# Kernel optimization log

Measured on AMD Instinct MI355X. Metric: run time of the kernel, lower is better.

The kernel has to match this reference:

```python
import jax, jax.numpy as jnp
import numpy as np
from jax import lax

B, T, D, E, N, P, S, NCLS, NBLK = 64, 16384, 128, 256, 8, 16, 1024, 18, 3
EPS = 1e-5


def setup_inputs() -> dict:
    key = jax.random.key(0)
    ks = jax.random.split(key, 20)
    inp = {
        'inputs': jax.random.normal(ks[0], (B, T, 6), jnp.float32),
        'acc_w': jax.random.normal(ks[1], (D // 2, 3, P), jnp.float32) * 0.1,
        'acc_b': jnp.zeros((D // 2,), jnp.float32),
        'gyro_w': jax.random.normal(ks[2], (D // 2, 3, P), jnp.float32) * 0.1,
        'gyro_b': jnp.zeros((D // 2,), jnp.float32),
        'pos_emb': jax.random.normal(ks[3], (S, D), jnp.float32),
        'ln_g': jnp.ones((NBLK, D), jnp.float32),
        'ln_b': jnp.zeros((NBLK, D), jnp.float32),
        'pc1_w': jax.random.normal(ks[4], (NBLK, E, D), jnp.float32) * 0.05,
        'pc1_b': jnp.zeros((NBLK, E), jnp.float32),
        'dw_w': jax.random.normal(ks[5], (NBLK, E, 5), jnp.float32) * 0.1,
        'dw_b': jnp.zeros((NBLK, E), jnp.float32),
        'bn_g': jnp.ones((NBLK, E), jnp.float32),
        'bn_b': jnp.zeros((NBLK, E), jnp.float32),
        'bn_mean': jnp.zeros((NBLK, E), jnp.float32),
        'bn_var': jnp.ones((NBLK, E), jnp.float32),
        'Ap': -0.5 * jnp.ones((NBLK, E), jnp.float32),
        'Bp': jax.random.normal(ks[6], (NBLK, E, N), jnp.float32) * 0.1,
        'Cp': jax.random.normal(ks[7], (NBLK, E, N), jnp.float32) * 0.1,
        'Dp': jax.random.normal(ks[8], (NBLK, E), jnp.float32) * 0.1,
        'pc2_w': jax.random.normal(ks[9], (NBLK, D, E), jnp.float32) * 0.05,
        'pc2_b': jnp.zeros((NBLK, D), jnp.float32),
        'fln_g': jnp.ones((D,), jnp.float32),
        'fln_b': jnp.zeros((D,), jnp.float32),
        'hw1': jax.random.normal(ks[10], (D, 2 * D), jnp.float32) * 0.05,
        'hb1': jnp.zeros((2 * D,), jnp.float32),
        'hw2': jax.random.normal(ks[11], (2 * D, NCLS), jnp.float32) * 0.05,
        'hb2': jnp.zeros((NCLS,), jnp.float32),
    }
    return inp


def _layernorm(x, g, b):
    m = x.mean(-1, keepdims=True)
    v = ((x - m) ** 2).mean(-1, keepdims=True)
    return (x - m) * lax.rsqrt(v + EPS) * g + b


def _conv1d(x, w, b, stride):
    # x [B,C,L], w [O,I,K]
    y = lax.conv_general_dilated(x, w, (stride,), 'VALID',
                                 dimension_numbers=('NCH', 'OIH', 'NCH'))
    return y + b[None, :, None]


def _mamba(x, pc1_w, pc1_b, dw_w, dw_b, bn_g, bn_b, bn_mean, bn_var,
           Ap, Bp, Cp, Dp, pc2_w, pc2_b):
    # x: [B,S,D]
    xc = jax.nn.silu(jnp.einsum('bsd,ed->bse', x, pc1_w) + pc1_b)  # [B,S,E]
    xt = jnp.swapaxes(xc, 1, 2)  # [B,E,S]
    # depthwise conv k=5, pad=2, groups=E
    xl = lax.conv_general_dilated(xt, dw_w[:, None, :], (1,), [(2, 2)],
                                  feature_group_count=E,
                                  dimension_numbers=('NCH', 'OIH', 'NCH'))
    xl = xl + dw_b[None, :, None]
    # BatchNorm1d (eval mode, running stats)
    scale = bn_g * lax.rsqrt(bn_var + EPS)
    xl = (xl - bn_mean[None, :, None]) * scale[None, :, None] + bn_b[None, :, None]
    xl = jax.nn.silu(xl)
    x_local = jnp.swapaxes(xl, 1, 2)  # [B,S,E]
    # SSM scan: h = exp(A)*h + x_t * B ; y = sum(C*h) + D*x_t
    A_exp = jnp.exp(Ap)  # [E]

    def step(h, xt_):
        # h [B,E,N], xt_ [B,E]
        h = A_exp[None, :, None] * h + xt_[..., None] * Bp[None]
        y = jnp.einsum('ben,en->be', h, Cp) + Dp * xt_
        return h, y

    h0 = jnp.zeros((x_local.shape[0], E, N), x_local.dtype)
    _, ys = lax.scan(step, h0, jnp.swapaxes(x_local, 0, 1))  # ys [S,B,E]
    out = jnp.swapaxes(ys, 0, 1)  # [B,S,E]
    out = jnp.einsum('bse,de->bsd', out, pc2_w) + pc2_b
    return out


def reference(inputs, acc_w, acc_b, gyro_w, gyro_b, pos_emb,
              ln_g, ln_b, pc1_w, pc1_b, dw_w, dw_b, bn_g, bn_b, bn_mean, bn_var,
              Ap, Bp, Cp, Dp, pc2_w, pc2_b, fln_g, fln_b, hw1, hb1, hw2, hb2):
    acc = jnp.swapaxes(inputs[:, :, :3], 1, 2)   # [B,3,T]
    gyro = jnp.swapaxes(inputs[:, :, 3:], 1, 2)  # [B,3,T]
    acc_p = jnp.swapaxes(_conv1d(acc, acc_w, acc_b, 16), 1, 2)    # [B,S,D/2]
    gyro_p = jnp.swapaxes(_conv1d(gyro, gyro_w, gyro_b, 16), 1, 2)
    x = jnp.concatenate([acc_p, gyro_p], axis=2)  # [B,S,D]
    x = x + pos_emb[None]
    for i in range(NBLK):
        y = _layernorm(x, ln_g[i], ln_b[i])
        y = _mamba(y, pc1_w[i], pc1_b[i], dw_w[i], dw_b[i], bn_g[i], bn_b[i],
                   bn_mean[i], bn_var[i], Ap[i], Bp[i], Cp[i], Dp[i],
                   pc2_w[i], pc2_b[i])
        x = y + x
    x = _layernorm(x, fln_g, fln_b)
    x = x.mean(axis=1)  # [B,D]
    h = jax.nn.silu(x @ hw1 + hb1)
    logits = h @ hw2 + hb2
    return jax.nn.softmax(logits, axis=-1)
```

## Files before the change

kernel.cpp:

```cpp
#include <hip/hip_runtime.h>
#include <hip/hip_bf16.h>

#define BB 64
#define TT 16384
#define DD 128
#define EE 256
#define NN 8
#define SS 1024
#define NCLS 18
#define NBLK 3
#define EPSV 1e-5f

typedef __bf16 bf16x8 __attribute__((ext_vector_type(8)));
typedef __bf16 bf16x4 __attribute__((ext_vector_type(4)));
typedef float f32x4 __attribute__((ext_vector_type(4)));
typedef unsigned short ushort_t;

__device__ __forceinline__ float silu_f(float z) {
    return z * __builtin_amdgcn_rcpf(1.0f + __expf(-z));
}
__device__ __forceinline__ unsigned int bfbits(float v) {
    return (unsigned int)__builtin_bit_cast(unsigned short, (__bf16)v);
}
__device__ __forceinline__ float bflow(unsigned int u) {
    return (float)__builtin_bit_cast(__bf16, (unsigned short)(u & 0xffffu));
}
__device__ __forceinline__ float bfhigh(unsigned int u) {
    return (float)__builtin_bit_cast(__bf16, (unsigned short)(u >> 16));
}

__global__ __launch_bounds__(256) void k_pack(
    const float* __restrict__ w1, const float* __restrict__ w2,
    const float* __restrict__ dw_w, const float* __restrict__ dw_b,
    const float* __restrict__ bn_g, const float* __restrict__ bn_b,
    const float* __restrict__ bn_mean, const float* __restrict__ bn_var,
    const float* __restrict__ Ap, const float* __restrict__ Bp,
    const float* __restrict__ Cp, const float* __restrict__ Dp,
    ushort_t* __restrict__ wpk1, ushort_t* __restrict__ wpk2,
    float* __restrict__ sparm) {
    const int t0 = blockIdx.x * 256 + threadIdx.x;
    if (t0 >= 24576) {
        const int t = t0 - 24576;
        if (t >= 768) return;
        const int le = t;
        const float scale = bn_g[le] * rsqrtf(bn_var[le] + EPSV);
        float cb = 0.0f;
#pragma unroll
        for (int n = 0; n < 8; ++n) cb += Cp[le * 8 + n] * Bp[le * 8 + n];
        float* dst = sparm + (size_t)le * 12;
        dst[0] = dw_w[le * 5 + 0] * scale;
        dst[1] = dw_w[le * 5 + 1] * scale;
        dst[2] = dw_w[le * 5 + 2] * scale;
        dst[3] = dw_w[le * 5 + 3] * scale;
        dst[4] = dw_w[le * 5 + 4] * scale;
        dst[5] = (dw_b[le] - bn_mean[le]) * scale + bn_b[le];
        dst[6] = __expf(Ap[le]);
        dst[7] = cb;
        dst[8] = Dp[le];
        dst[9] = 0.0f; dst[10] = 0.0f; dst[11] = 0.0f;
        return;
    }
    const float* src;
    uint4* dst;
    if (t0 < 12288) {
        const int L = t0 >> 12;
        const int r = t0 & 4095;
        const int ks = r >> 10;
        const int r2 = r & 1023;
        const int nf = r2 >> 6;
        const int lane = r2 & 63;
        const int col = nf * 16 + (lane & 15);
        const int k0 = ks * 32 + (lane >> 4) * 8;
        src = w1 + ((size_t)L * EE + col) * DD + k0;
        dst = (uint4*)wpk1 + t0;
    } else {
        const int t = t0 - 12288;
        const int L = t >> 12;
        const int r = t & 4095;
        const int ks = r >> 9;
        const int r2 = r & 511;
        const int nf = r2 >> 6;
        const int lane = r2 & 63;
        const int col = nf * 16 + (lane & 15);
        const int k0 = ks * 32 + (lane >> 4) * 8;
        src = w2 + ((size_t)L * DD + col) * EE + k0;
        dst = (uint4*)wpk2 + t;
    }
    const float4 a = ((const float4*)src)[0];
    const float4 b = ((const float4*)src)[1];
    bf16x8 pk;
    pk[0] = (__bf16)a.x; pk[1] = (__bf16)a.y; pk[2] = (__bf16)a.z; pk[3] = (__bf16)a.w;
    pk[4] = (__bf16)b.x; pk[5] = (__bf16)b.y; pk[6] = (__bf16)b.z; pk[7] = (__bf16)b.w;
    *dst = __builtin_bit_cast(uint4, pk);
}

__device__ __forceinline__ void xt_store(ushort_t* xt16, int row, int col,
                                         ushort_t val) {
    xt16[row * 128 + (((col >> 3) ^ (row & 7)) << 3) + (col & 7)] = val;
}

template <int MROWS, int NT>
__device__ __forceinline__ void ln_pc1_tail(
    char* smem, const int tid,
    const float* __restrict__ lng, const float* __restrict__ lnb,
    const ushort_t* __restrict__ wpk, const float* __restrict__ bias1,
    __bf16* __restrict__ xcT, const int bidx, const int sg0) {
    constexpr int TPR = NT / MROWS;
    constexpr int CPT = 16 / TPR;
    const uint4* xt = (const uint4*)smem;
    uint4* A2 = (uint4*)(smem + MROWS * 256);

    {
        const int row = tid / TPR;
        const int q = tid % TPR;
        float v[CPT * 8];
#pragma unroll
        for (int i = 0; i < CPT; ++i) {
            const uint4 tv4 = xt[row * 16 + ((q * CPT + i) ^ (row & 7))];
            const bf16x8 tv = __builtin_bit_cast(bf16x8, tv4);
#pragma unroll
            for (int e2 = 0; e2 < 8; ++e2) v[i * 8 + e2] = (float)tv[e2];
        }
        float s1 = 0.0f, s2 = 0.0f;
#pragma unroll
        for (int i = 0; i < CPT * 8; ++i) { s1 += v[i]; s2 += v[i] * v[i]; }
        s1 += __shfl_xor(s1, 1); s2 += __shfl_xor(s2, 1);
        s1 += __shfl_xor(s1, 2); s2 += __shfl_xor(s2, 2);
        const float mean = s1 * (1.0f / 128.0f);
        const float rstd = rsqrtf(s2 * (1.0f / 128.0f) - mean * mean + EPSV);
        const float4* gp4 = (const float4*)lng;
        const float4* bp4 = (const float4*)lnb;
#pragma unroll
        for (int c = 0; c < CPT; ++c) {
            const int ci = q * CPT + c;
            float4 g0 = gp4[ci * 2], g1 = gp4[ci * 2 + 1];
            float4 b0 = bp4[ci * 2], b1 = bp4[ci * 2 + 1];
            const float gg[8] = {g0.x, g0.y, g0.z, g0.w, g1.x, g1.y, g1.z, g1.w};
            const float bb2[8] = {b0.x, b0.y, b0.z, b0.w, b1.x, b1.y, b1.z, b1.w};
            bf16x8 pk;
#pragma unroll
            for (int e2 = 0; e2 < 8; ++e2)
                pk[e2] = (__bf16)((v[c * 8 + e2] - mean) * rstd * gg[e2] + bb2[e2]);
            A2[(row * 16 + ci) ^ (row & 7)] = __builtin_bit_cast(uint4, pk);
        }
    }
    __syncthreads();

    const int wv = tid >> 6;
    const int wr = wv >> 2;
    const int wc = wv & 3;
    const int lane = tid & 63;
    const int lrow = lane & 15;
    const int lk = lane >> 4;
    const uint4* wq = (const uint4*)wpk;

    f32x4 acc[4][4] = {};
    for (int ks = 0; ks < 4; ++ks) {
        bf16x8 av[4], bw[4];
#pragma unroll
        for (int m = 0; m < 4; ++m) {
            const int row = wr * 64 + m * 16 + lrow;
            const int idx = (row * 16 + ks * 4 + lk) ^ (row & 7);
            av[m] = __builtin_bit_cast(bf16x8, A2[idx]);
        }
#pragma unroll
        for (int n = 0; n < 4; ++n) {
            const int nf = wc * 4 + n;
            bw[n] = __builtin_bit_cast(bf16x8, wq[(ks * 16 + nf) * 64 + lane]);
        }
#pragma unroll
        for (int m = 0; m < 4; ++m)
#pragma unroll
            for (int n = 0; n < 4; ++n)
                acc[m][n] = __builtin_amdgcn_mfma_f32_16x16x32_bf16(av[m], bw[n], acc[m][n], 0, 0, 0);
    }

#pragma unroll
    for (int n = 0; n < 4; ++n) {
        const int col = wc * 64 + n * 16 + lrow;
        const float bv = bias1[col];
#pragma unroll
        for (int m = 0; m < 4; ++m) {
            bf16x4 pk;
#pragma unroll
            for (int r = 0; r < 4; ++r)
                pk[r] = (__bf16)silu_f(acc[m][n][r] + bv);
            const int sg = sg0 + wr * 8 + m * 2 + (lk >> 1);
            __bf16* dst = xcT + ((((size_t)bidx * 128 + sg) * EE + col) << 3) +
                          (lk & 1) * 4;
            *(bf16x4*)dst = pk;
        }
    }
}

__global__ __launch_bounds__(256) void k_stem_mfma(
    const float* __restrict__ in, const float* __restrict__ acc_w,
    const float* __restrict__ acc_b, const float* __restrict__ gyro_w,
    const float* __restrict__ gyro_b, const float* __restrict__ pos_emb,
    __bf16* __restrict__ x,
    const float* __restrict__ lng, const float* __restrict__ lnb,
    const ushort_t* __restrict__ wpk1, const float* __restrict__ pc1b,
    __bf16* __restrict__ xcT) {
    __shared__ __align__(16) char smem[49152];
    uint4* Wl = (uint4*)smem;
    uint4* Al = (uint4*)(smem + 32768);

    const int tid = threadIdx.x;
    const int rbase = blockIdx.x * 64;
    const int b = rbase >> 10;
    const int sbase = rbase & 1023;

    if (tid < 128) {
        const int d = tid;
        const float* wsrc = (d < 64) ? (acc_w + d * 48) : (gyro_w + (d - 64) * 48);
        float aw[48];
        const float4* wq4 = (const float4*)wsrc;
#pragma unroll
        for (int q = 0; q < 12; ++q) {
            float4 t = wq4[q];
            aw[q * 4 + 0] = t.x; aw[q * 4 + 1] = t.y;
            aw[q * 4 + 2] = t.z; aw[q * 4 + 3] = t.w;
        }
        const bool isacc = (d < 64);
#pragma unroll
        for (int cc = 0; cc < 12; ++cc) {
            unsigned int wb[8];
#pragma unroll
            for (int e = 0; e < 8; ++e) {
                const int j = cc * 8 + e;
                const int p = j / 6, rem = j % 6;
                float val;
                if (rem < 3) val = isacc ? aw[rem * 16 + p] : 0.0f;
                else         val = isacc ? 0.0f : aw[(rem - 3) * 16 + p];
                wb[e] = bfbits(val);
            }
            uint4 pk;
            pk.x = wb[0] | (wb[1] << 16);
            pk.y = wb[2] | (wb[3] << 16);
            pk.z = wb[4] | (wb[5] << 16);
            pk.w = wb[6] | (wb[7] << 16);
            Wl[d * 16 + (cc ^ (d & 7))] = pk;
        }
    }

    {
        const float* abase = in + (size_t)b * (TT * 6) + (size_t)sbase * 96;
#pragma unroll
        for (int it = 0; it < 3; ++it) {
            const int idx = it * 256 + tid;
            const int row = idx / 12;
            const int ch = idx % 12;
            const float* src = abase + row * 96 + ch * 8;
            const float4 t0 = *(const float4*)src;
            const float4 t1 = *(const float4*)(src + 4);
            uint4 pk;
            pk.x = bfbits(t0.x) | (bfbits(t0.y) << 16);
            pk.y = bfbits(t0.z) | (bfbits(t0.w) << 16);
            pk.z = bfbits(t1.x) | (bfbits(t1.y) << 16);
            pk.w = bfbits(t1.z) | (bfbits(t1.w) << 16);
            Al[row * 16 + (ch ^ (row & 7))] = pk;
        }
    }
    __syncthreads();

    const int wv = tid >> 6;
    const int lane = tid & 63;
    const int lrow = lane & 15;
    const int lk = lane >> 4;

    f32x4 acc[4][2] = {};
#pragma unroll
    for (int ks = 0; ks < 3; ++ks) {
        bf16x8 a[4], bf[2];
#pragma unroll
        for (int m = 0; m < 4; ++m) {
            const int row = m * 16 + lrow;
            a[m] = __builtin_bit_cast(bf16x8, Al[row * 16 + ((ks * 4 + lk) ^ (row & 7))]);
        }
#pragma unroll
        for (int n = 0; n < 2; ++n) {
            const int col = (wv * 2 + n) * 16 + lrow;
            bf[n] = __builtin_bit_cast(bf16x8, Wl[col * 16 + ((ks * 4 + lk) ^ (col & 7))]);
        }
#pragma unroll
        for (int m = 0; m < 4; ++m)
#pragma unroll
            for (int n = 0; n < 2; ++n)
                acc[m][n] = __builtin_amdgcn_mfma_f32_16x16x32_bf16(a[m], bf[n], acc[m][n], 0, 0, 0);
    }
    __syncthreads();

    ushort_t* xt16 = (ushort_t*)smem;
#pragma unroll
    for (int n = 0; n < 2; ++n) {
        const int col = (wv * 2 + n) * 16 + lrow;
        const float bv = (col < 64) ? acc_b[col] : gyro_b[col - 64];
#pragma unroll
        for (int m = 0; m < 4; ++m)
#pragma unroll
            for (int r = 0; r < 4; ++r) {
                const int row = m * 16 + lk * 4 + r;
                const float pe = pos_emb[(size_t)(sbase + row) * DD + col];
                const float xv = acc[m][n][r] + bv + pe;
                xt_store(xt16, row, col, __builtin_bit_cast(ushort_t, (__bf16)xv));
            }
    }
    __syncthreads();

    {
        uint4* xg = (uint4*)x;
        const uint4* xt4 = (const uint4*)smem;
#pragma unroll
        for (int k = 0; k < 4; ++k) {
            const int idx = k * 256 + tid;
            const int row = idx >> 4;
            const int ch = idx & 15;
            xg[((size_t)(rbase + row) << 4) + ch] = xt4[row * 16 + (ch ^ (row & 7))];
        }
    }
    ln_pc1_tail<64, 256>(smem, tid, lng, lnb, wpk1, pc1b, xcT, b, sbase >> 3);
}

template <int TAIL>
__global__ __launch_bounds__(512, 4) void k_scan_pc2(
    const __bf16* __restrict__ xcIn,
    const ushort_t* __restrict__ wpk2_,
    const float* __restrict__ sparm,
    const float* __restrict__ bias, __bf16* __restrict__ x,
    const float* __restrict__ lng, const float* __restrict__ lnb,
    const ushort_t* __restrict__ wpk1, const float* __restrict__ pc1b,
    __bf16* __restrict__ xcOut) {
    __shared__ __align__(16) char smem[65536];

    const int tid = threadIdx.x;
    const int sc = blockIdx.x;
    const int b = blockIdx.y;

    {
        const int e = tid & 255;
        const int sub = tid >> 8;
        const int sce = sc * 2 + sub;
        const float4 p0 = *(const float4*)(sparm + (size_t)e * 12);
        const float4 p1 = *(const float4*)(sparm + (size_t)e * 12 + 4);
        const float Dv = sparm[(size_t)e * 12 + 8];
        const float d0 = p0.x, d1 = p0.y, d2 = p0.z, d3 = p0.w;
        const float d4 = p1.x, cbias = p1.y, Aexp = p1.z, cb = p1.w;

        const int sgbase = sce * 8 - 4;
        const uint4* xq = (const uint4*)xcIn + ((size_t)b * 128 + sgbase) * EE + e;
        uint4 G[13];
#pragma unroll
        for (int j = 0; j < 13; ++j) {
            const int sg = sgbase + j;
            G[j] = (sg >= 0 && sg < 128) ? xq[j * EE] : make_uint4(0, 0, 0, 0);
        }

        __bf16* lbase = (__bf16*)smem;
        const int ehash = e >> 3;
        const int elow = e & 7;
        const int rowoff = sub * 64;

        float g = 0.0f, pw6, pw7;
        if (sce != 0) {
            pw6 = bflow(G[0].w); pw7 = bfhigh(G[0].w);
#pragma unroll
            for (int j = 1; j <= 3; ++j) {
                float cw[8];
                cw[0] = bflow(G[j].x); cw[1] = bfhigh(G[j].x);
                cw[2] = bflow(G[j].y); cw[3] = bfhigh(G[j].y);
                cw[4] = bflow(G[j].z); cw[5] = bfhigh(G[j].z);
                cw[6] = bflow(G[j].w); cw[7] = bfhigh(G[j].w);
                const float nh0 = bflow(G[j + 1].x);
                const float nh1 = bfhigh(G[j + 1].x);
#pragma unroll
                for (int u = 0; u < 8; ++u) {
                    const float xm2 = (u >= 2) ? cw[u - 2] : (u == 0 ? pw6 : pw7);
                    const float xm1 = (u >= 1) ? cw[u - 1] : pw7;
                    const float x0 = cw[u];
                    const float xp1 = (u < 7) ? cw[u + 1] : nh0;
                    const float xp2 = (u < 6) ? cw[u + 2] : (u == 6 ? nh0 : nh1);
                    const float z = xm2 * d0 + xm1 * d1 + x0 * d2 + xp1 * d3 +
                                    xp2 * d4 + cbias;
                    g = fmaf(Aexp, g, silu_f(z));
                }
                pw6 = cw[6]; pw7 = cw[7];
            }
        } else {
            pw6 = 0.0f; pw7 = 0.0f;
        }

#pragma unroll
        for (int j = 4; j <= 11; ++j) {
            float cw[8];
            cw[0] = bflow(G[j].x); cw[1] = bfhigh(G[j].x);
            cw[2] = bflow(G[j].y); cw[3] = bfhigh(G[j].y);
            cw[4] = bflow(G[j].z); cw[5] = bfhigh(G[j].z);
            cw[6] = bflow(G[j].w); cw[7] = bfhigh(G[j].w);
            const float nh0 = bflow(G[j + 1].x);
            const float nh1 = bfhigh(G[j + 1].x);

            float aa[8];
#pragma unroll
            for (int u = 0; u < 8; ++u) {
                const float xm2 = (u >= 2) ? cw[u - 2] : (u == 0 ? pw6 : pw7);
                const float xm1 = (u >= 1) ? cw[u - 1] : pw7;
                const float x0 = cw[u];
                const float xp1 = (u < 7) ? cw[u + 1] : nh0;
                const float xp2 = (u < 6) ? cw[u + 2] : (u == 6 ? nh0 : nh1);
                const float z = xm2 * d0 + xm1 * d1 + x0 * d2 + xp1 * d3 +
                                xp2 * d4 + cbias;
                aa[u] = silu_f(z);
            }
#pragma unroll
            for (int u = 0; u < 8; ++u) {
                g = fmaf(Aexp, g, aa[u]);
                const int r = rowoff + (j - 4) * 8 + u;
                lbase[r * 256 + ((ehash ^ (r & 7)) << 3) + elow] =
                    (__bf16)(cb * g + Dv * aa[u]);
            }
            pw6 = cw[6]; pw7 = cw[7];
        }
    }
    __syncthreads();

    const int wv = tid >> 6;
    const int wr = wv >> 2;
    const int wc = wv & 3;
    const int lane = tid & 63;
    const int lrow = lane & 15;
    const int lk = lane >> 4;
    const uint4* wq = (const uint4*)wpk2_;
    const uint4* Albd = (const uint4*)smem;

    f32x4 acc[4][2] = {};
    for (int ks = 0; ks < 8; ++ks) {
        bf16x8 a[4], bfr[2];
#pragma unroll
        for (int m = 0; m < 4; ++m) {
            const int row = wr * 64 + m * 16 + lrow;
            const int idx = (row * 32 + ks * 4 + lk) ^ (row & 7);
            a[m] = __builtin_bit_cast(bf16x8, Albd[idx]);
        }
#pragma unroll
        for (int n = 0; n < 2; ++n) {
            const int nf = wc * 2 + n;
            bfr[n] = __builtin_bit_cast(bf16x8, wq[(ks * 8 + nf) * 64 + lane]);
        }
#pragma unroll
        for (int m = 0; m < 4; ++m)
#pragma unroll
            for (int n = 0; n < 2; ++n)
                acc[m][n] = __builtin_amdgcn_mfma_f32_16x16x32_bf16(a[m], bfr[n], acc[m][n], 0, 0, 0);
    }
    __syncthreads();

    {
        float* y2f = (float*)smem;
#pragma unroll
        for (int n = 0; n < 2; ++n) {
            const int col = wc * 32 + n * 16 + lrow;
            const float bv = bias[col];
#pragma unroll
            for (int m = 0; m < 4; ++m)
#pragma unroll
                for (int r = 0; r < 4; ++r) {
                    const int row = wr * 64 + m * 16 + lk * 4 + r;
                    y2f[row * 128 + (col ^ ((row & 7) << 2))] = acc[m][n][r] + bv;
                }
        }
    }
    __syncthreads();

    const size_t rbase = ((size_t)b << 10) + ((size_t)sc << 7);
    uint4 newx[4];
    {
        const uint4* y24 = (const uint4*)smem;
        uint4* xg = (uint4*)x;
#pragma unroll
        for (int k = 0; k < 4; ++k) {
            const int idx = k * 512 + tid;
            const int row = idx >> 4;
            const int ch = idx & 15;
            const f32x4 ya = __builtin_bit_cast(f32x4, y24[row * 32 + ((ch * 2) ^ (row & 7))]);
            const f32x4 yb = __builtin_bit_cast(f32x4, y24[row * 32 + ((ch * 2 + 1) ^ (row & 7))]);
            const bf16x8 xo = __builtin_bit_cast(bf16x8, xg[((rbase + row) << 4) + ch]);
            bf16x8 pk;
#pragma unroll
            for (int e2 = 0; e2 < 4; ++e2) {
                pk[e2] = (__bf16)((float)xo[e2] + ya[e2]);
                pk[e2 + 4] = (__bf16)((float)xo[e2 + 4] + yb[e2]);
            }
            newx[k] = __builtin_bit_cast(uint4, pk);
            xg[((rbase + row) << 4) + ch] = newx[k];
        }
    }

    if constexpr (TAIL) {
        __syncthreads();
        uint4* xt4 = (uint4*)smem;
#pragma unroll
        for (int k = 0; k < 4; ++k) {
            const int idx = k * 512 + tid;
            const int row = idx >> 4;
            const int ch = idx & 15;
            xt4[row * 16 + (ch ^ (row & 7))] = newx[k];
        }
        __syncthreads();
        ln_pc1_tail<128, 512>(smem, tid, lng, lnb, wpk1, pc1b, xcOut, b, sc * 16);
    }
}

__global__ __launch_bounds__(256) void k_finln_s1(
    const __bf16* __restrict__ x, float* __restrict__ partial) {
    const int chunk = blockIdx.x;
    const int b = blockIdx.y;
    const int tid = threadIdx.x;
    const int wv = tid >> 6;
    const int lane = tid & 63;
    const __bf16* xb = x + ((size_t)b * SS + chunk * 128) * DD;

    float a0 = 0.0f, a1 = 0.0f;
    for (int s = wv; s < 128; s += 4) {
        const unsigned int vv = *(const unsigned int*)(xb + (size_t)s * DD + lane * 2);
        const float vx = bflow(vv);
        const float vy = bfhigh(vv);
        float s1 = vx + vy;
        float s2 = vx * vx + vy * vy;
#pragma unroll
        for (int m = 1; m <= 32; m <<= 1) {
            s1 += __shfl_xor(s1, m);
            s2 += __shfl_xor(s2, m);
        }
        const float mean = s1 * (1.0f / 128.0f);
        const float rstd = rsqrtf(s2 * (1.0f / 128.0f) - mean * mean + EPSV);
        a0 += (vx - mean) * rstd;
        a1 += (vy - mean) * rstd;
    }
    __shared__ float red[4][128];
    red[wv][lane * 2] = a0;
    red[wv][lane * 2 + 1] = a1;
    __syncthreads();
    if (tid < 128) {
        partial[((size_t)b * 8 + chunk) * 128 + tid] =
            red[0][tid] + red[1][tid] + red[2][tid] + red[3][tid];
    }
}

__global__ __launch_bounds__(256) void k_head(
    const float* __restrict__ partial, const float* __restrict__ fg,
    const float* __restrict__ fb, const float* __restrict__ hw1,
    const float* __restrict__ hb1, const float* __restrict__ hw2,
    const float* __restrict__ hb2, float* __restrict__ out) {
    const int b = blockIdx.x;
    const int tid = threadIdx.x;
    __shared__ float xmb[128];
    __shared__ float hh[256];
    __shared__ float lg[18];
    __shared__ float eg[18];

    if (tid < 128) {
        float s = 0.0f;
#pragma unroll
        for (int c = 0; c < 8; ++c)
            s += partial[((size_t)b * 8 + c) * 128 + tid];
        xmb[tid] = fg[tid] * (s * (1.0f / (float)SS)) + fb[tid];
    }
    __syncthreads();

    float z = hb1[tid];
    for (int k = 0; k < 128; ++k) z += xmb[k] * hw1[k * 256 + tid];
    hh[tid] = z / (1.0f + expf(-z));
    __syncthreads();

    if (tid < NCLS) {
        float a = hb2[tid];
        for (int k = 0; k < 256; ++k) a += hh[k] * hw2[k * NCLS + tid];
        lg[tid] = a;
    }
    __syncthreads();
    if (tid < NCLS) {
        float m = lg[0];
        for (int j = 1; j < NCLS; ++j) m = fmaxf(m, lg[j]);
        eg[tid] = expf(lg[tid] - m);
    }
    __syncthreads();
    if (tid < NCLS) {
        float ssum = 0.0f;
        for (int j = 0; j < NCLS; ++j) ssum += eg[j];
        out[b * NCLS + tid] = eg[tid] / ssum;
    }
}

extern "C" void kernel_launch(void* const* d_in, const int* in_sizes, int n_in,
                              void* d_out, int out_size, void* d_ws, size_t ws_size,
                              hipStream_t stream) {
    const float* inputs  = (const float*)d_in[0];
    const float* acc_w   = (const float*)d_in[1];
    const float* acc_b   = (const float*)d_in[2];
    const float* gyro_w  = (const float*)d_in[3];
    const float* gyro_b  = (const float*)d_in[4];
    const float* pos_emb = (const float*)d_in[5];
    const float* ln_g    = (const float*)d_in[6];
    const float* ln_b    = (const float*)d_in[7];
    const float* pc1_w   = (const float*)d_in[8];
    const float* pc1_b   = (const float*)d_in[9];
    const float* dw_w    = (const float*)d_in[10];
    const float* dw_b    = (const float*)d_in[11];
    const float* bn_g    = (const float*)d_in[12];
    const float* bn_b    = (const float*)d_in[13];
    const float* bn_mean = (const float*)d_in[14];
    const float* bn_var  = (const float*)d_in[15];
    const float* Ap      = (const float*)d_in[16];
    const float* Bp      = (const float*)d_in[17];
    const float* Cp      = (const float*)d_in[18];
    const float* Dp      = (const float*)d_in[19];
    const float* pc2_w   = (const float*)d_in[20];
    const float* pc2_b   = (const float*)d_in[21];
    const float* fln_g   = (const float*)d_in[22];
    const float* fln_b   = (const float*)d_in[23];
    const float* hw1     = (const float*)d_in[24];
    const float* hb1     = (const float*)d_in[25];
    const float* hw2     = (const float*)d_in[26];
    const float* hb2     = (const float*)d_in[27];

    const size_t nx  = (size_t)BB * SS * DD;
    const size_t nxc = (size_t)BB * SS * EE;

    ushort_t* wsu = (ushort_t*)d_ws;
    ushort_t* xb   = wsu;
    ushort_t* xc0  = xb + nx;
    ushort_t* xc1  = xc0 + nxc;
    ushort_t* wpk1 = xc1 + nxc;
    ushort_t* wpk2 = wpk1 + 3 * 32768;
    float* sparm   = (float*)(wpk2 + 3 * 32768);
    float* partial = sparm + 3 * 256 * 12;

    __bf16* x    = (__bf16*)xb;
    __bf16* xcT0 = (__bf16*)xc0;
    __bf16* xcT1 = (__bf16*)xc1;

    k_pack<<<99, 256, 0, stream>>>(pc1_w, pc2_w, dw_w, dw_b, bn_g, bn_b,
                                   bn_mean, bn_var, Ap, Bp, Cp, Dp,
                                   wpk1, wpk2, sparm);

    k_stem_mfma<<<1024, 256, 0, stream>>>(inputs, acc_w, acc_b, gyro_w, gyro_b,
                                          pos_emb, x,
                                          ln_g, ln_b, wpk1, pc1_b, xcT0);

    k_scan_pc2<1><<<dim3(8, BB), 512, 0, stream>>>(
        xcT0, wpk2, sparm,
        pc2_b, x,
        ln_g + DD, ln_b + DD, wpk1 + 32768, pc1_b + EE, xcT1);

    k_scan_pc2<1><<<dim3(8, BB), 512, 0, stream>>>(
        xcT1, wpk2 + 32768, sparm + 256 * 12,
        pc2_b + DD, x,
        ln_g + 2 * DD, ln_b + 2 * DD, wpk1 + 2 * 32768, pc1_b + 2 * EE, xcT0);

    k_scan_pc2<0><<<dim3(8, BB), 512, 0, stream>>>(
        xcT0, wpk2 + 2 * 32768, sparm + 2 * 256 * 12,
        pc2_b + 2 * DD, x,
        nullptr, nullptr, nullptr, nullptr, nullptr);

    k_finln_s1<<<dim3(8, BB), 256, 0, stream>>>(x, partial);
    k_head<<<BB, 256, 0, stream>>>(partial, fln_g, fln_b, hw1, hb1, hw2, hb2,
                                   (float*)d_out);
}
```

Measured before the change: 154.9 us.

## Stream scan inputs through LDS with global_load_lds instead of register preload

Replaces the upfront register preload of 13 uint4 values per thread with a one-ahead pipeline. Each step loads into a per-wave LDS staging slot via global_load_lds and reads back the previous slot. Out-of-range rows point to a zeroed global buffer initialised in the pack kernel. This cuts register pressure in the scan stage but serialises global latency with vmcnt(0) waits and adds 8KB of shared memory per block.

```diff
diff --git a/kernel.cpp b/kernel.cpp
--- a/kernel.cpp
+++ b/kernel.cpp
@@ -28,6 +28,11 @@
 __device__ __forceinline__ float bfhigh(unsigned int u) {
     return (float)__builtin_bit_cast(__bf16, (unsigned short)(u >> 16));
 }
+__device__ __forceinline__ void gload_lds16(const void* g, void* l) {
+    __builtin_amdgcn_global_load_lds(
+        (const __attribute__((address_space(1))) unsigned*)g,
+        (__attribute__((address_space(3))) unsigned*)l, 16, 0, 0);
+}
 
 __global__ __launch_bounds__(256) void k_pack(
     const float* __restrict__ w1, const float* __restrict__ w2,
@@ -37,8 +42,9 @@
     const float* __restrict__ Ap, const float* __restrict__ Bp,
     const float* __restrict__ Cp, const float* __restrict__ Dp,
     ushort_t* __restrict__ wpk1, ushort_t* __restrict__ wpk2,
-    float* __restrict__ sparm) {
+    float* __restrict__ sparm, float* __restrict__ zbuf) {
     const int t0 = blockIdx.x * 256 + threadIdx.x;
+    if (t0 < 1024) zbuf[t0] = 0.0f;
     if (t0 >= 24576) {
         const int t = t0 - 24576;
         if (t >= 768) return;
@@ -329,8 +335,8 @@
     const float* __restrict__ bias, __bf16* __restrict__ x,
     const float* __restrict__ lng, const float* __restrict__ lnb,
     const ushort_t* __restrict__ wpk1, const float* __restrict__ pc1b,
-    __bf16* __restrict__ xcOut) {
-    __shared__ __align__(16) char smem[65536];
+    __bf16* __restrict__ xcOut, const uint4* __restrict__ zbuf) {
+    __shared__ __align__(16) char smem[73728];
 
     const int tid = threadIdx.x;
     const int sc = blockIdx.x;
@@ -340,6 +346,8 @@
         const int e = tid & 255;
         const int sub = tid >> 8;
         const int sce = sc * 2 + sub;
+        const int lane = tid & 63;
+        const int wvid = tid >> 6;
         const float4 p0 = *(const float4*)(sparm + (size_t)e * 12);
         const float4 p1 = *(const float4*)(sparm + (size_t)e * 12 + 4);
         const float Dv = sparm[(size_t)e * 12 + 8];
@@ -348,30 +356,78 @@
 
         const int sgbase = sce * 8 - 4;
         const uint4* xq = (const uint4*)xcIn + ((size_t)b * 128 + sgbase) * EE + e;
-        uint4 G[13];
-#pragma unroll
-        for (int j = 0; j < 13; ++j) {
-            const int sg = sgbase + j;
-            G[j] = (sg >= 0 && sg < 128) ? xq[j * EE] : make_uint4(0, 0, 0, 0);
-        }
+        char* stg = smem + 65536 + wvid * 1024;
 
         __bf16* lbase = (__bf16*)smem;
         const int ehash = e >> 3;
         const int elow = e & 7;
         const int rowoff = sub * 64;
 
+        {
+            const int sg = sgbase;
+            const void* gp = (sg >= 0 && sg < 128) ? (const void*)xq
+                                                   : (const void*)(zbuf + lane);
+            gload_lds16(gp, stg);
+        }
+        asm volatile("s_waitcnt vmcnt(0)" ::: "memory");
+        uint4 Gc = *(const uint4*)(stg + lane * 16);
+        asm volatile("" ::"v"(Gc.x), "v"(Gc.y), "v"(Gc.z), "v"(Gc.w) : "memory");
+        {
+            const int sg = sgbase + 1;
+            const void* gp = (sg >= 0 && sg < 128) ? (const void*)(xq + EE)
+                                                   : (const void*)(zbuf + lane);
+            gload_lds16(gp, stg);
+        }
+
         float g = 0.0f, pw6, pw7;
-        if (sce != 0) {
-            pw6 = bflow(G[0].w); pw7 = bfhigh(G[0].w);
-#pragma unroll
-            for (int j = 1; j <= 3; ++j) {
+        if (sce != 0) { pw6 = bflow(Gc.w); pw7 = bfhigh(Gc.w); }
+        else          { pw6 = 0.0f;        pw7 = 0.0f; }
+
+#pragma unroll
+        for (int j = 1; j <= 12; ++j) {
+            asm volatile("s_waitcnt vmcnt(0)" ::: "memory");
+            const uint4 Gn = *(const uint4*)(stg + lane * 16);
+            asm volatile("" ::"v"(Gn.x), "v"(Gn.y), "v"(Gn.z), "v"(Gn.w) : "memory");
+            if (j < 12) {
+                const int sg = sgbase + j + 1;
+                const void* gp = (sg >= 0 && sg < 128)
+                                     ? (const void*)(xq + (size_t)(j + 1) * EE)
+                                     : (const void*)(zbuf + lane);
+                gload_lds16(gp, stg);
+            }
+            const int gj = j - 1;
+            if (gj >= 1 && gj <= 3) {
+                if (sce != 0) {
+                    float cw[8];
+                    cw[0] = bflow(Gc.x); cw[1] = bfhigh(Gc.x);
+                    cw[2] = bflow(Gc.y); cw[3] = bfhigh(Gc.y);
+                    cw[4] = bflow(Gc.z); cw[5] = bfhigh(Gc.z);
+                    cw[6] = bflow(Gc.w); cw[7] = bfhigh(Gc.w);
+                    const float nh0 = bflow(Gn.x);
+                    const float nh1 = bfhigh(Gn.x);
+#pragma unroll
+                    for (int u = 0; u < 8; ++u) {
+                        const float xm2 = (u >= 2) ? cw[u - 2] : (u == 0 ? pw6 : pw7);
+                        const float xm1 = (u >= 1) ? cw[u - 1] : pw7;
+                        const float x0 = cw[u];
+                        const float xp1 = (u < 7) ? cw[u + 1] : nh0;
+                        const float xp2 = (u < 6) ? cw[u + 2] : (u == 6 ? nh0 : nh1);
+                        const float z = xm2 * d0 + xm1 * d1 + x0 * d2 + xp1 * d3 +
+                                        xp2 * d4 + cbias;
+                        g = fmaf(Aexp, g, silu_f(z));
+                    }
+                    pw6 = cw[6]; pw7 = cw[7];
+                }
+            } else if (gj >= 4) {
                 float cw[8];
-                cw[0] = bflow(G[j].x); cw[1] = bfhigh(G[j].x);
-                cw[2] = bflow(G[j].y); cw[3] = bfhigh(G[j].y);
-                cw[4] = bflow(G[j].z); cw[5] = bfhigh(G[j].z);
-                cw[6] = bflow(G[j].w); cw[7] = bfhigh(G[j].w);
-                const float nh0 = bflow(G[j + 1].x);
-                const float nh1 = bfhigh(G[j + 1].x);
+                cw[0] = bflow(Gc.x); cw[1] = bfhigh(Gc.x);
+                cw[2] = bflow(Gc.y); cw[3] = bfhigh(Gc.y);
+                cw[4] = bflow(Gc.z); cw[5] = bfhigh(Gc.z);
+                cw[6] = bflow(Gc.w); cw[7] = bfhigh(Gc.w);
+                const float nh0 = bflow(Gn.x);
+                const float nh1 = bfhigh(Gn.x);
+
+                float aa[8];
 #pragma unroll
                 for (int u = 0; u < 8; ++u) {
                     const float xm2 = (u >= 2) ? cw[u - 2] : (u == 0 ? pw6 : pw7);
@@ -381,44 +437,18 @@
                     const float xp2 = (u < 6) ? cw[u + 2] : (u == 6 ? nh0 : nh1);
                     const float z = xm2 * d0 + xm1 * d1 + x0 * d2 + xp1 * d3 +
                                     xp2 * d4 + cbias;
-                    g = fmaf(Aexp, g, silu_f(z));
+                    aa[u] = silu_f(z);
+                }
+#pragma unroll
+                for (int u = 0; u < 8; ++u) {
+                    g = fmaf(Aexp, g, aa[u]);
+                    const int r = rowoff + (gj - 4) * 8 + u;
+                    lbase[r * 256 + ((ehash ^ (r & 7)) << 3) + elow] =
+                        (__bf16)(cb * g + Dv * aa[u]);
                 }
                 pw6 = cw[6]; pw7 = cw[7];
             }
-        } else {
-            pw6 = 0.0f; pw7 = 0.0f;
-        }
-
-#pragma unroll
-        for (int j = 4; j <= 11; ++j) {
-            float cw[8];
-            cw[0] = bflow(G[j].x); cw[1] = bfhigh(G[j].x);
-            cw[2] = bflow(G[j].y); cw[3] = bfhigh(G[j].y);
-            cw[4] = bflow(G[j].z); cw[5] = bfhigh(G[j].z);
-            cw[6] = bflow(G[j].w); cw[7] = bfhigh(G[j].w);
-            const float nh0 = bflow(G[j + 1].x);
-            const float nh1 = bfhigh(G[j + 1].x);
-
-            float aa[8];
-#pragma unroll
-            for (int u = 0; u < 8; ++u) {
-                const float xm2 = (u >= 2) ? cw[u - 2] : (u == 0 ? pw6 : pw7);
-                const float xm1 = (u >= 1) ? cw[u - 1] : pw7;
-                const float x0 = cw[u];
-                const float xp1 = (u < 7) ? cw[u + 1] : nh0;
-                const float xp2 = (u < 6) ? cw[u + 2] : (u == 6 ? nh0 : nh1);
-                const float z = xm2 * d0 + xm1 * d1 + x0 * d2 + xp1 * d3 +
-                                xp2 * d4 + cbias;
-                aa[u] = silu_f(z);
-            }
-#pragma unroll
-            for (int u = 0; u < 8; ++u) {
-                g = fmaf(Aexp, g, aa[u]);
-                const int r = rowoff + (j - 4) * 8 + u;
-                lbase[r * 256 + ((ehash ^ (r & 7)) << 3) + elow] =
-                    (__bf16)(cb * g + Dv * aa[u]);
-            }
-            pw6 = cw[6]; pw7 = cw[7];
+            Gc = Gn;
         }
     }
     __syncthreads();
@@ -634,14 +664,16 @@
     ushort_t* wpk2 = wpk1 + 3 * 32768;
     float* sparm   = (float*)(wpk2 + 3 * 32768);
     float* partial = sparm + 3 * 256 * 12;
+    float* zbuf    = partial + (size_t)BB * 8 * 128;
 
     __bf16* x    = (__bf16*)xb;
     __bf16* xcT0 = (__bf16*)xc0;
     __bf16* xcT1 = (__bf16*)xc1;
+    const uint4* zb4 = (const uint4*)zbuf;
 
     k_pack<<<99, 256, 0, stream>>>(pc1_w, pc2_w, dw_w, dw_b, bn_g, bn_b,
                                    bn_mean, bn_var, Ap, Bp, Cp, Dp,
-                                   wpk1, wpk2, sparm);
+                                   wpk1, wpk2, sparm, zbuf);
 
     k_stem_mfma<<<1024, 256, 0, stream>>>(inputs, acc_w, acc_b, gyro_w, gyro_b,
                                           pos_emb, x,
@@ -650,17 +682,17 @@
     k_scan_pc2<1><<<dim3(8, BB), 512, 0, stream>>>(
         xcT0, wpk2, sparm,
         pc2_b, x,
-        ln_g + DD, ln_b + DD, wpk1 + 32768, pc1_b + EE, xcT1);
+        ln_g + DD, ln_b + DD, wpk1 + 32768, pc1_b + EE, xcT1, zb4);
 
     k_scan_pc2<1><<<dim3(8, BB), 512, 0, stream>>>(
         xcT1, wpk2 + 32768, sparm + 256 * 12,
         pc2_b + DD, x,
-        ln_g + 2 * DD, ln_b + 2 * DD, wpk1 + 2 * 32768, pc1_b + 2 * EE, xcT0);
+        ln_g + 2 * DD, ln_b + 2 * DD, wpk1 + 2 * 32768, pc1_b + 2 * EE, xcT0, zb4);
 
     k_scan_pc2<0><<<dim3(8, BB), 512, 0, stream>>>(
         xcT0, wpk2 + 2 * 32768, sparm + 2 * 256 * 12,
         pc2_b + 2 * DD, x,
-        nullptr, nullptr, nullptr, nullptr, nullptr);
+        nullptr, nullptr, nullptr, nullptr, nullptr, zb4);
 
     k_finln_s1<<<dim3(8, BB), 256, 0, stream>>>(x, partial);
     k_head<<<BB, 256, 0, stream>>>(partial, fln_g, fln_b, hw1, hb1, hw2, hb2,
```

Measured after the change: 154.8 us. About the same (-0.1%).
